# Optimization experiments

Hardware: AMD Instinct MI355X
Metric: run time of the kernel (lower is better)

Reference implementation:

```python
import jax, jax.numpy as jnp
import numpy as np

EMBED = 1024
HEADS = 16
HEAD_DIM = EMBED // HEADS


def setup_inputs() -> dict:
    key = jax.random.key(0)
    ks = jax.random.split(key, 12)
    B, S, D = 4, 2048, EMBED
    scale = 1.0 / np.sqrt(D)
    inp = {
        "query": jax.random.normal(ks[0], (B, S, D), dtype=jnp.float32),
        "key": jax.random.normal(ks[1], (B, S, D), dtype=jnp.float32),
        "value": jax.random.normal(ks[2], (B, S, D), dtype=jnp.float32),
        "Wq": jax.random.normal(ks[3], (D, D), dtype=jnp.float32) * scale,
        "bq": jnp.zeros((D,), dtype=jnp.float32),
        "Wk": jax.random.normal(ks[4], (D, D), dtype=jnp.float32) * scale,
        "bk": jnp.zeros((D,), dtype=jnp.float32),
        "Wv": jax.random.normal(ks[5], (D, D), dtype=jnp.float32) * scale,
        "bv": jnp.zeros((D,), dtype=jnp.float32),
        "Wo": jax.random.normal(ks[6], (D, D), dtype=jnp.float32) * scale,
        "bo": jnp.zeros((D,), dtype=jnp.float32),
    }
    return inp


def reference(query, key, value, Wq, bq, Wk, bk, Wv, bv, Wo, bo):
    B, S, D = query.shape
    H, Dh = HEADS, HEAD_DIM

    def proj(x, W, b):
        # nn.Linear: x @ W.T + b, then split heads -> [B, H, S, Dh]
        y = jnp.einsum('bsd,ed->bse', x, W) + b
        return y.reshape(B, -1, H, Dh).transpose(0, 2, 1, 3)

    q = proj(query, Wq, bq)
    k = proj(key, Wk, bk)
    v = proj(value, Wv, bv)

    attn = jnp.einsum('bhqd,bhkd->bhqk', q, k) / jnp.sqrt(jnp.float32(Dh))
    attn = jax.nn.softmax(attn, axis=-1)
    # dropout: eval mode -> identity
    out = jnp.einsum('bhqk,bhkd->bhqd', attn, v)
    out = out.transpose(0, 2, 1, 3).reshape(B, -1, D)
    out = jnp.einsum('bsd,ed->bse', out, Wo) + bo
    return out
```

## Files before the change

### kernel.cpp

```cpp
#include <hip/hip_runtime.h>
#include <hip/hip_bf16.h>

typedef unsigned short u16;
typedef unsigned int u32;
typedef float f32x4 __attribute__((ext_vector_type(4)));
typedef float f32x16 __attribute__((ext_vector_type(16)));
typedef __bf16 bf16x8 __attribute__((ext_vector_type(8)));
typedef u32 u32x2 __attribute__((ext_vector_type(2)));

#define DEV static __device__ __forceinline__

DEV u16 f2b(float f) { __bf16 h = (__bf16)f; u16 r; __builtin_memcpy(&r, &h, 2); return r; }
DEV u32 pk2(float a, float b) { return (u32)f2b(a) | ((u32)f2b(b) << 16); }
DEV bf16x8 as_bf(uint4 v) { bf16x8 r; __builtin_memcpy(&r, &v, 16); return r; }

#define GLDS(g, l) __builtin_amdgcn_global_load_lds( \
    (__attribute__((address_space(1))) void*)(g),     \
    (__attribute__((address_space(3))) void*)(l), 16, 0, 0)

DEV void wb2() { asm volatile("s_waitcnt vmcnt(2)\n\ts_barrier" ::: "memory"); }
DEV void wb0() { asm volatile("s_waitcnt vmcnt(0)\n\ts_barrier" ::: "memory"); }

__global__ __launch_bounds__(256) void conva_k(const float* __restrict__ src,
                                               u16* __restrict__ dst, int n8)
{
  int i = blockIdx.x * 256 + threadIdx.x;
  const int stride = gridDim.x * 256;
  for (; i < n8; i += stride) {
    const float4* p = (const float4*)(src + (size_t)i * 8);
    const float4 a = p[0], b = p[1];
    *(uint4*)(dst + (size_t)i * 8) =
        make_uint4(pk2(a.x, a.y), pk2(a.z, a.w), pk2(b.x, b.y), pk2(b.z, b.w));
  }
}

__global__ __launch_bounds__(256) void convw_k(const float* __restrict__ w0,
                                               const float* __restrict__ w1,
                                               const float* __restrict__ w2,
                                               const float* __restrict__ w3,
                                               u16* __restrict__ dst)
{
  const int seg = blockIdx.x >> 9, sb = blockIdx.x & 511;
  const float* s = seg == 0 ? w0 : seg == 1 ? w1 : seg == 2 ? w2 : w3;
  const int i = sb * 256 + threadIdx.x;
  const float4* p = (const float4*)(s + (size_t)i * 8);
  const float4 a = p[0], b = p[1];
  *(uint4*)(dst + (size_t)seg * 1048576 + (size_t)i * 8) =
      make_uint4(pk2(a.x, a.y), pk2(a.z, a.w), pk2(b.x, b.y), pk2(b.z, b.w));
}

template<int CMODE>
__global__ __launch_bounds__(512, 4) void gemm_b(const u16* __restrict__ A,
                                                 const u16* __restrict__ W,
                                                 const float* __restrict__ bias,
                                                 void* __restrict__ Cp, float scale)
{
  __shared__ u16 lds[3][8192];
  const int tid = threadIdx.x;
  const int lane = tid & 63, w = tid >> 6;
  const int m0 = blockIdx.x * 128, e0 = blockIdx.y * 128;
  const int wrb = (w >> 1) * 2, wcb = (w & 1) * 4;

  f32x4 acc[2][4];
#pragma unroll
  for (int i = 0; i < 2; i++)
#pragma unroll
    for (int j = 0; j < 4; j++)
#pragma unroll
      for (int r = 0; r < 4; r++) acc[i][j][r] = 0.f;

  const u16* gA = A + (size_t)(m0 + w * 16 + (lane & 15)) * 1024 + (lane >> 4) * 8;
  const u16* gB = W + (size_t)(e0 + w * 16 + (lane & 15)) * 1024 + (lane >> 4) * 8;

  GLDS(gA,      &lds[0][w * 512]);
  GLDS(gB,      &lds[0][4096 + w * 512]);
  GLDS(gA + 32, &lds[1][w * 512]);
  GLDS(gB + 32, &lds[1][4096 + w * 512]);

  u16 *rc = &lds[0][0], *rn = &lds[1][0], *rf = &lds[2][0];
  const int fo = (lane >> 4) * 128 + (lane & 15) * 8;

#define GEMM_STEP(KL)                                                          \
  {                                                                            \
    const u16* la = (KL);                                                      \
    const u16* lb = (KL) + 4096;                                               \
    bf16x8 af[2], bfr[4];                                                      \
    _Pragma("unroll")                                                          \
    for (int i = 0; i < 2; i++)                                                \
      af[i] = as_bf(*(const uint4*)(la + (wrb + i) * 512 + fo));               \
    _Pragma("unroll")                                                          \
    for (int j = 0; j < 4; j++)                                                \
      bfr[j] = as_bf(*(const uint4*)(lb + (wcb + j) * 512 + fo));              \
    _Pragma("unroll")                                                          \
    for (int i = 0; i < 2; i++)                                                \
      _Pragma("unroll")                                                        \
      for (int j = 0; j < 4; j++)                                              \
        acc[i][j] = __builtin_amdgcn_mfma_f32_16x16x32_bf16(af[i], bfr[j],     \
                                                            acc[i][j], 0, 0, 0); \
  }

  for (int kb = 0; kb < 31; ++kb) {
    wb2();
    if (kb < 30) {
      GLDS(gA + (kb + 2) * 32, rf + w * 512);
      GLDS(gB + (kb + 2) * 32, rf + 4096 + w * 512);
    }
    GEMM_STEP(rc)
    u16* tmp = rc; rc = rn; rn = rf; rf = tmp;
  }
  wb0();
  GEMM_STEP(rc)
#undef GEMM_STEP

  const int col = lane & 15, rb4 = (lane >> 4) * 4;
  const int wr = wrb * 16, wc = wcb * 16;
#pragma unroll
  for (int j = 0; j < 4; j++) {
    const int e = e0 + wc + j * 16 + col;
    const float bv = bias[e];
#pragma unroll
    for (int i = 0; i < 2; i++) {
#pragma unroll
      for (int r = 0; r < 4; r++) {
        const int m = m0 + wr + i * 16 + rb4 + r;
        const float v = (acc[i][j][r] + bv) * scale;
        if (CMODE == 0) {
          ((float*)Cp)[(size_t)m * 1024 + e] = v;
        } else {
          const int b = m >> 11, s = m & 2047, h = e >> 6, dh = e & 63;
          const size_t bh = (size_t)(b * 16 + h);
          if (CMODE == 2) {
            const size_t idx = (((bh * 64 + (s >> 5)) * 4 + (dh >> 4)) * 64
                                + ((dh >> 3) & 1) * 32 + (s & 31)) * 8 + (dh & 7);
            ((u16*)Cp)[idx] = f2b(v);
          } else {
            const size_t idx = ((bh * 64 + (s >> 5)) * 8 + ((s >> 4) & 1) * 4
                                + (dh >> 5) * 2 + ((s >> 3) & 1)) * 256
                               + (size_t)(dh & 31) * 8 + (s & 7);
            ((u16*)Cp)[idx] = f2b(v);
          }
        }
      }
    }
  }
}

__global__ __launch_bounds__(256, 4) void attn_k(const u16* __restrict__ Qb,
                                                 const u16* __restrict__ Kb,
                                                 const u16* __restrict__ Vb,
                                                 u16* __restrict__ O)
{
  __shared__ u16 pool[12288];
  const int tid = threadIdx.x, wv = tid >> 6, lane = tid & 63;
  const int lo = lane & 31, hi = lane >> 5;
  const int bid = blockIdx.x;
  const int xcd = bid & 7, ix = bid >> 3;
  const int bh = xcd * 8 + (ix & 7);
  const int qb = (ix >> 3) * 4 + wv;
  const int b = bh >> 4, h = bh & 15, q0 = qb * 32;

  const u16* qp = Qb + ((size_t)(bh * 64 + qb) * 4) * 512 + (size_t)lane * 8;
  bf16x8 qf[4];
#pragma unroll
  for (int c = 0; c < 4; c++) qf[c] = as_bf(*(const uint4*)(qp + c * 512));

  const uint4 onesw = make_uint4(0x3F803F80u, 0x3F803F80u, 0x3F803F80u, 0x3F803F80u);
  const bf16x8 ones = as_bf(onesw);

  f32x16 a0, a1, a2, zv;
#pragma unroll
  for (int r = 0; r < 16; r++) { a0[r] = 0.f; a1[r] = 0.f; a2[r] = 0.f; zv[r] = 0.f; }

  const u16* sgK = Kb + (size_t)bh * 131072 + wv * 512 + (size_t)lane * 8;
  const u16* sgV = Vb + (size_t)bh * 131072 + wv * 512 + (size_t)lane * 8;

  GLDS(sgK,        pool + wv * 512);
  GLDS(sgV,        pool + 2048 + wv * 512);
  GLDS(sgK + 2048, pool + 4096 + wv * 512);
  GLDS(sgV + 2048, pool + 4096 + 2048 + wv * 512);

  u16 *rc = pool, *rn = pool + 4096, *rf = pool + 8192;

#define ATTN_STEP(KL)                                                         \
  {                                                                           \
    const u16* kl = (KL);                                                     \
    const u16* vl = (KL) + 2048;                                              \
    __builtin_amdgcn_s_setprio(1);                                            \
    f32x16 s = __builtin_amdgcn_mfma_f32_32x32x16_bf16(                       \
                 as_bf(*(const uint4*)(kl + lane * 8)), qf[0], zv, 0, 0, 0);  \
    _Pragma("unroll")                                                         \
    for (int c = 1; c < 4; c++)                                               \
      s = __builtin_amdgcn_mfma_f32_32x32x16_bf16(                            \
            as_bf(*(const uint4*)(kl + c * 512 + lane * 8)), qf[c], s, 0, 0, 0); \
    __builtin_amdgcn_s_setprio(0);                                            \
    _Pragma("unroll")                                                         \
    for (int r = 0; r < 16; r++) s[r] = __builtin_amdgcn_exp2f(s[r]);         \
    bf16x8 pf[2];                                                             \
    _Pragma("unroll")                                                         \
    for (int kc = 0; kc < 2; kc++) {                                          \
      const u32 A0 = pk2(s[8 * kc + 0], s[8 * kc + 1]);                       \
      const u32 A1 = pk2(s[8 * kc + 2], s[8 * kc + 3]);                       \
      const u32 B0 = pk2(s[8 * kc + 4], s[8 * kc + 5]);                       \
      const u32 B1 = pk2(s[8 * kc + 6], s[8 * kc + 7]);                       \
      u32x2 w02 = __builtin_amdgcn_permlane32_swap(A0, B0, false, false);     \
      u32x2 w13 = __builtin_amdgcn_permlane32_swap(A1, B1, false, false);     \
      pf[kc] = as_bf(make_uint4(w02[0], w13[0], w02[1], w13[1]));             \
    }                                                                         \
    __builtin_amdgcn_s_setprio(1);                                            \
    a0 = __builtin_amdgcn_mfma_f32_32x32x16_bf16(                             \
           as_bf(*(const uint4*)(vl + 0    + lane * 8)), pf[0], a0, 0, 0, 0); \
    a1 = __builtin_amdgcn_mfma_f32_32x32x16_bf16(                             \
           as_bf(*(const uint4*)(vl + 512  + lane * 8)), pf[0], a1, 0, 0, 0); \
    a2 = __builtin_amdgcn_mfma_f32_32x32x16_bf16(ones, pf[0], a2, 0, 0, 0);   \
    a0 = __builtin_amdgcn_mfma_f32_32x32x16_bf16(                             \
           as_bf(*(const uint4*)(vl + 1024 + lane * 8)), pf[1], a0, 0, 0, 0); \
    a1 = __builtin_amdgcn_mfma_f32_32x32x16_bf16(                             \
           as_bf(*(const uint4*)(vl + 1536 + lane * 8)), pf[1], a1, 0, 0, 0); \
    a2 = __builtin_amdgcn_mfma_f32_32x32x16_bf16(ones, pf[1], a2, 0, 0, 0);   \
    __builtin_amdgcn_s_setprio(0);                                            \
  }

  for (int t = 0; t < 63; ++t) {
    wb2();
    if (t < 62) {
      GLDS(sgK + (size_t)(t + 2) * 2048, rf + wv * 512);
      GLDS(sgV + (size_t)(t + 2) * 2048, rf + 2048 + wv * 512);
    }
    ATTN_STEP(rc)
    u16* tmp = rc; rc = rn; rn = rf; rf = tmp;
  }
  wb0();
  ATTN_STEP(rc)
#undef ATTN_STEP

  __syncthreads();

  const float inv = 1.f / a2[0];
  u16* ob = pool + (wv * 32) * 72;

#pragma unroll
  for (int r = 0; r < 16; r++) {
    const int dh = (r & 3) + 8 * (r >> 2) + 4 * hi;
    ob[lo * 72 + dh]      = f2b(a0[r] * inv);
    ob[lo * 72 + dh + 32] = f2b(a1[r] * inv);
  }
  __builtin_amdgcn_s_barrier();
  const int qr = lane >> 1, hf = lane & 1;
  const u16* src = ob + qr * 72 + hf * 32;
  const uint4 r0 = *(const uint4*)(src + 0);
  const uint4 r1 = *(const uint4*)(src + 8);
  const uint4 r2 = *(const uint4*)(src + 16);
  const uint4 r3 = *(const uint4*)(src + 24);
  const size_t m = (size_t)b * 2048 + q0 + qr;
  uint4* dst = (uint4*)(O + m * 1024 + (size_t)h * 64 + hf * 32);
  dst[0] = r0; dst[1] = r1; dst[2] = r2; dst[3] = r3;
}

extern "C" void kernel_launch(void* const* d_in, const int* in_sizes, int n_in,
                              void* d_out, int out_size, void* d_ws, size_t ws_size,
                              hipStream_t stream)
{
  const float* query = (const float*)d_in[0];
  const float* key   = (const float*)d_in[1];
  const float* value = (const float*)d_in[2];
  const float* Wq = (const float*)d_in[3];
  const float* bq = (const float*)d_in[4];
  const float* Wk = (const float*)d_in[5];
  const float* bk = (const float*)d_in[6];
  const float* Wv = (const float*)d_in[7];
  const float* bv = (const float*)d_in[8];
  const float* Wo = (const float*)d_in[9];
  const float* bo = (const float*)d_in[10];

  const size_t MAT = (size_t)8192 * 1024;
  const size_t WMAT = (size_t)1024 * 1024;
  if (ws_size < (4 * MAT + 4 * WMAT) * sizeof(u16)) return;
  u16* Ac = (u16*)d_ws;
  u16* Wc = Ac + MAT;
  u16* Qw = Wc + 4 * WMAT;
  u16* Kw = Qw + MAT;
  u16* Vw = Kw + MAT;
  u16* Ow = Ac;

  const float qscale = 0.125f * 1.4426950408889634f;

  dim3 bl(256, 1, 1), bg(512, 1, 1), gg(64, 8);
  hipLaunchKernelGGL(convw_k, dim3(2048), bl, 0, stream, Wq, Wk, Wv, Wo, Wc);

  hipLaunchKernelGGL(conva_k, dim3(2048), bl, 0, stream, query, Ac, (int)(MAT / 8));
  hipLaunchKernelGGL((gemm_b<2>), gg, bg, 0, stream, Ac, Wc + 0 * WMAT, bq, (void*)Qw, qscale);

  hipLaunchKernelGGL(conva_k, dim3(2048), bl, 0, stream, key, Ac, (int)(MAT / 8));
  hipLaunchKernelGGL((gemm_b<2>), gg, bg, 0, stream, Ac, Wc + 1 * WMAT, bk, (void*)Kw, 1.0f);

  hipLaunchKernelGGL(conva_k, dim3(2048), bl, 0, stream, value, Ac, (int)(MAT / 8));
  hipLaunchKernelGGL((gemm_b<3>), gg, bg, 0, stream, Ac, Wc + 2 * WMAT, bv, (void*)Vw, 1.0f);

  hipLaunchKernelGGL(attn_k, dim3(1024), bl, 0, stream, Qw, Kw, Vw, Ow);

  hipLaunchKernelGGL((gemm_b<0>), gg, bg, 0, stream, Ow, Wc + 3 * WMAT, bo, d_out, 1.0f);
}
```

Before: 262.8 us.

## Use 4-wave GEMM with larger per-wave tiles and drop ones-MFMA row sum

```diff
diff --git a/kernel.cpp b/kernel.cpp
--- a/kernel.cpp
+++ b/kernel.cpp
@@ -19,6 +19,7 @@
     (__attribute__((address_space(3))) void*)(l), 16, 0, 0)
 
 DEV void wb2() { asm volatile("s_waitcnt vmcnt(2)\n\ts_barrier" ::: "memory"); }
+DEV void wb4() { asm volatile("s_waitcnt vmcnt(4)\n\ts_barrier" ::: "memory"); }
 DEV void wb0() { asm volatile("s_waitcnt vmcnt(0)\n\ts_barrier" ::: "memory"); }
 
 __global__ __launch_bounds__(256) void conva_k(const float* __restrict__ src,
@@ -50,67 +51,66 @@
 }
 
 template<int CMODE>
-__global__ __launch_bounds__(512, 4) void gemm_b(const u16* __restrict__ A,
-                                                 const u16* __restrict__ W,
-                                                 const float* __restrict__ bias,
-                                                 void* __restrict__ Cp, float scale)
+__global__ __launch_bounds__(256) void gemm_b(const u16* __restrict__ A,
+                                              const u16* __restrict__ W,
+                                              const float* __restrict__ bias,
+                                              void* __restrict__ Cp, float scale)
 {
   __shared__ u16 lds[3][8192];
   const int tid = threadIdx.x;
   const int lane = tid & 63, w = tid >> 6;
   const int m0 = blockIdx.x * 128, e0 = blockIdx.y * 128;
-  const int wrb = (w >> 1) * 2, wcb = (w & 1) * 4;
-
-  f32x4 acc[2][4];
-#pragma unroll
-  for (int i = 0; i < 2; i++)
+  const int wrb = (w >> 1) * 4, wcb = (w & 1) * 4;
+
+  f32x4 acc[4][4];
+#pragma unroll
+  for (int i = 0; i < 4; i++)
 #pragma unroll
     for (int j = 0; j < 4; j++)
 #pragma unroll
       for (int r = 0; r < 4; r++) acc[i][j][r] = 0.f;
 
-  const u16* gA = A + (size_t)(m0 + w * 16 + (lane & 15)) * 1024 + (lane >> 4) * 8;
-  const u16* gB = W + (size_t)(e0 + w * 16 + (lane & 15)) * 1024 + (lane >> 4) * 8;
-
-  GLDS(gA,      &lds[0][w * 512]);
-  GLDS(gB,      &lds[0][4096 + w * 512]);
-  GLDS(gA + 32, &lds[1][w * 512]);
-  GLDS(gB + 32, &lds[1][4096 + w * 512]);
-
-  u16 *rc = &lds[0][0], *rn = &lds[1][0], *rf = &lds[2][0];
+  const u16* gA = A + (size_t)(m0 + w * 32 + (lane & 15)) * 1024 + (lane >> 4) * 8;
+  const u16* gB = W + (size_t)(e0 + w * 32 + (lane & 15)) * 1024 + (lane >> 4) * 8;
+
+#define GSTAGE(K0, BUF)                                        \
+  GLDS(gA + (K0),         &lds[BUF][w * 1024]);                \
+  GLDS(gA + (K0) + 16384, &lds[BUF][w * 1024 + 512]);          \
+  GLDS(gB + (K0),         &lds[BUF][4096 + w * 1024]);         \
+  GLDS(gB + (K0) + 16384, &lds[BUF][4096 + w * 1024 + 512]);
+
+  GSTAGE(0, 0)
+  GSTAGE(32, 1)
+
   const int fo = (lane >> 4) * 128 + (lane & 15) * 8;
 
-#define GEMM_STEP(KL)                                                          \
+#define GEMM_STEP(BUF)                                                         \
   {                                                                            \
-    const u16* la = (KL);                                                      \
-    const u16* lb = (KL) + 4096;                                               \
-    bf16x8 af[2], bfr[4];                                                      \
+    const u16* la = &lds[BUF][0];                                              \
+    const u16* lb = &lds[BUF][4096];                                           \
+    bf16x8 af[4], bfr[4];                                                      \
     _Pragma("unroll")                                                          \
-    for (int i = 0; i < 2; i++)                                                \
-      af[i] = as_bf(*(const uint4*)(la + (wrb + i) * 512 + fo));               \
+    for (int i = 0; i < 4; i++) {                                              \
+      af[i]  = as_bf(*(const uint4*)(la + (wrb + i) * 512 + fo));              \
+      bfr[i] = as_bf(*(const uint4*)(lb + (wcb + i) * 512 + fo));              \
+    }                                                                          \
     _Pragma("unroll")                                                          \
-    for (int j = 0; j < 4; j++)                                                \
-      bfr[j] = as_bf(*(const uint4*)(lb + (wcb + j) * 512 + fo));              \
-    _Pragma("unroll")                                                          \
-    for (int i = 0; i < 2; i++)                                                \
+    for (int i = 0; i < 4; i++)                                                \
       _Pragma("unroll")                                                        \
       for (int j = 0; j < 4; j++)                                              \
         acc[i][j] = __builtin_amdgcn_mfma_f32_16x16x32_bf16(af[i], bfr[j],     \
                                                             acc[i][j], 0, 0, 0); \
   }
 
-  for (int kb = 0; kb < 31; ++kb) {
-    wb2();
-    if (kb < 30) {
-      GLDS(gA + (kb + 2) * 32, rf + w * 512);
-      GLDS(gB + (kb + 2) * 32, rf + 4096 + w * 512);
-    }
-    GEMM_STEP(rc)
-    u16* tmp = rc; rc = rn; rn = rf; rf = tmp;
-  }
-  wb0();
-  GEMM_STEP(rc)
+  for (int t = 0; t < 30; t += 3) {
+    wb4(); GSTAGE((t + 2) * 32, 2) GEMM_STEP(0)
+    wb4(); GSTAGE((t + 3) * 32, 0) GEMM_STEP(1)
+    wb4(); GSTAGE((t + 4) * 32, 1) GEMM_STEP(2)
+  }
+  wb4(); GEMM_STEP(0)
+  wb0(); GEMM_STEP(1)
 #undef GEMM_STEP
+#undef GSTAGE
 
   const int col = lane & 15, rb4 = (lane >> 4) * 4;
   const int wr = wrb * 16, wc = wcb * 16;
@@ -119,7 +119,7 @@
     const int e = e0 + wc + j * 16 + col;
     const float bv = bias[e];
 #pragma unroll
-    for (int i = 0; i < 2; i++) {
+    for (int i = 0; i < 4; i++) {
 #pragma unroll
       for (int r = 0; r < 4; r++) {
         const int m = m0 + wr + i * 16 + rb4 + r;
@@ -164,27 +164,25 @@
 #pragma unroll
   for (int c = 0; c < 4; c++) qf[c] = as_bf(*(const uint4*)(qp + c * 512));
 
-  const uint4 onesw = make_uint4(0x3F803F80u, 0x3F803F80u, 0x3F803F80u, 0x3F803F80u);
-  const bf16x8 ones = as_bf(onesw);
-
-  f32x16 a0, a1, a2, zv;
-#pragma unroll
-  for (int r = 0; r < 16; r++) { a0[r] = 0.f; a1[r] = 0.f; a2[r] = 0.f; zv[r] = 0.f; }
+  f32x16 a0, a1, zv;
+#pragma unroll
+  for (int r = 0; r < 16; r++) { a0[r] = 0.f; a1[r] = 0.f; zv[r] = 0.f; }
+  float ls0 = 0.f, ls1 = 0.f;
 
   const u16* sgK = Kb + (size_t)bh * 131072 + wv * 512 + (size_t)lane * 8;
   const u16* sgV = Vb + (size_t)bh * 131072 + wv * 512 + (size_t)lane * 8;
 
-  GLDS(sgK,        pool + wv * 512);
-  GLDS(sgV,        pool + 2048 + wv * 512);
-  GLDS(sgK + 2048, pool + 4096 + wv * 512);
-  GLDS(sgV + 2048, pool + 4096 + 2048 + wv * 512);
-
-  u16 *rc = pool, *rn = pool + 4096, *rf = pool + 8192;
-
-#define ATTN_STEP(KL)                                                         \
+#define ASTAGE(T, BUF)                                                  \
+  GLDS(sgK + (size_t)(T) * 2048, pool + (BUF) * 4096 + wv * 512);       \
+  GLDS(sgV + (size_t)(T) * 2048, pool + (BUF) * 4096 + 2048 + wv * 512);
+
+  ASTAGE(0, 0)
+  ASTAGE(1, 1)
+
+#define ATTN_STEP(BUF)                                                        \
   {                                                                           \
-    const u16* kl = (KL);                                                     \
-    const u16* vl = (KL) + 2048;                                              \
+    const u16* kl = pool + (BUF) * 4096;                                      \
+    const u16* vl = kl + 2048;                                                \
     __builtin_amdgcn_s_setprio(1);                                            \
     f32x16 s = __builtin_amdgcn_mfma_f32_32x32x16_bf16(                       \
                  as_bf(*(const uint4*)(kl + lane * 8)), qf[0], zv, 0, 0, 0);  \
@@ -195,6 +193,8 @@
     __builtin_amdgcn_s_setprio(0);                                            \
     _Pragma("unroll")                                                         \
     for (int r = 0; r < 16; r++) s[r] = __builtin_amdgcn_exp2f(s[r]);         \
+    _Pragma("unroll")                                                         \
+    for (int r = 0; r < 16; r += 2) { ls0 += s[r]; ls1 += s[r + 1]; }         \
     bf16x8 pf[2];                                                             \
     _Pragma("unroll")                                                         \
     for (int kc = 0; kc < 2; kc++) {                                          \
@@ -211,31 +211,30 @@
            as_bf(*(const uint4*)(vl + 0    + lane * 8)), pf[0], a0, 0, 0, 0); \
     a1 = __builtin_amdgcn_mfma_f32_32x32x16_bf16(                             \
            as_bf(*(const uint4*)(vl + 512  + lane * 8)), pf[0], a1, 0, 0, 0); \
-    a2 = __builtin_amdgcn_mfma_f32_32x32x16_bf16(ones, pf[0], a2, 0, 0, 0);   \
     a0 = __builtin_amdgcn_mfma_f32_32x32x16_bf16(                             \
            as_bf(*(const uint4*)(vl + 1024 + lane * 8)), pf[1], a0, 0, 0, 0); \
     a1 = __builtin_amdgcn_mfma_f32_32x32x16_bf16(                             \
            as_bf(*(const uint4*)(vl + 1536 + lane * 8)), pf[1], a1, 0, 0, 0); \
-    a2 = __builtin_amdgcn_mfma_f32_32x32x16_bf16(ones, pf[1], a2, 0, 0, 0);   \
     __builtin_amdgcn_s_setprio(0);                                            \
   }
 
-  for (int t = 0; t < 63; ++t) {
-    wb2();
-    if (t < 62) {
-      GLDS(sgK + (size_t)(t + 2) * 2048, rf + wv * 512);
-      GLDS(sgV + (size_t)(t + 2) * 2048, rf + 2048 + wv * 512);
-    }
-    ATTN_STEP(rc)
-    u16* tmp = rc; rc = rn; rn = rf; rf = tmp;
-  }
-  wb0();
-  ATTN_STEP(rc)
+  for (int t = 0; t < 60; t += 3) {
+    wb2(); ASTAGE(t + 2, 2) ATTN_STEP(0)
+    wb2(); ASTAGE(t + 3, 0) ATTN_STEP(1)
+    wb2(); ASTAGE(t + 4, 1) ATTN_STEP(2)
+  }
+  wb2(); ASTAGE(62, 2) ATTN_STEP(0)
+  wb2(); ASTAGE(63, 0) ATTN_STEP(1)
+  wb2(); ATTN_STEP(2)
+  wb0(); ATTN_STEP(0)
 #undef ATTN_STEP
+#undef ASTAGE
 
   __syncthreads();
 
-  const float inv = 1.f / a2[0];
+  float l = ls0 + ls1;
+  l += __shfl_xor(l, 32);
+  const float inv = 1.f / l;
   u16* ob = pool + (wv * 32) * 72;
 
 #pragma unroll
@@ -284,19 +283,19 @@
 
   const float qscale = 0.125f * 1.4426950408889634f;
 
-  dim3 bl(256, 1, 1), bg(512, 1, 1), gg(64, 8);
+  dim3 bl(256, 1, 1), gg(64, 8);
   hipLaunchKernelGGL(convw_k, dim3(2048), bl, 0, stream, Wq, Wk, Wv, Wo, Wc);
 
   hipLaunchKernelGGL(conva_k, dim3(2048), bl, 0, stream, query, Ac, (int)(MAT / 8));
-  hipLaunchKernelGGL((gemm_b<2>), gg, bg, 0, stream, Ac, Wc + 0 * WMAT, bq, (void*)Qw, qscale);
+  hipLaunchKernelGGL((gemm_b<2>), gg, bl, 0, stream, Ac, Wc + 0 * WMAT, bq, (void*)Qw, qscale);
 
   hipLaunchKernelGGL(conva_k, dim3(2048), bl, 0, stream, key, Ac, (int)(MAT / 8));
-  hipLaunchKernelGGL((gemm_b<2>), gg, bg, 0, stream, Ac, Wc + 1 * WMAT, bk, (void*)Kw, 1.0f);
+  hipLaunchKernelGGL((gemm_b<2>), gg, bl, 0, stream, Ac, Wc + 1 * WMAT, bk, (void*)Kw, 1.0f);
 
   hipLaunchKernelGGL(conva_k, dim3(2048), bl, 0, stream, value, Ac, (int)(MAT / 8));
-  hipLaunchKernelGGL((gemm_b<3>), gg, bg, 0, stream, Ac, Wc + 2 * WMAT, bv, (void*)Vw, 1.0f);
+  hipLaunchKernelGGL((gemm_b<3>), gg, bl, 0, stream, Ac, Wc + 2 * WMAT, bv, (void*)Vw, 1.0f);
 
   hipLaunchKernelGGL(attn_k, dim3(1024), bl, 0, stream, Qw, Kw, Vw, Ow);
 
-  hipLaunchKernelGGL((gemm_b<0>), gg, bg, 0, stream, Ow, Wc + 3 * WMAT, bo, d_out, 1.0f);
-}
+  hipLaunchKernelGGL((gemm_b<0>), gg, bl, 0, stream, Ow, Wc + 3 * WMAT, bo, d_out, 1.0f);
+}
```

Result: no change. 262.9 us (+0.1%).
